# Optimization experiments

Measured on AMD Instinct MI355X. Metric: run time of the kernel, lower is better.

The kernel has to match this reference:

```python
import jax, jax.numpy as jnp
import numpy as np
from jax import lax

CAPACITY = 32768
KEY_SIZE = 64
VALUE_SIZE = 64
BATCH = 4096


def setup_inputs() -> dict:
    key = jax.random.key(0)
    ks = jax.random.split(key, 9)
    inp = {
        "keys": jax.random.normal(ks[0], (BATCH, KEY_SIZE), dtype=jnp.float32),
        "values": jax.random.normal(ks[1], (BATCH, VALUE_SIZE), dtype=jnp.float32),
        "query": jax.random.normal(ks[2], (BATCH, KEY_SIZE), dtype=jnp.float32),
        # learned memory tables (init as torch.randn * 0.01)
        "mem_keys": jax.random.normal(ks[3], (CAPACITY, KEY_SIZE), dtype=jnp.float32) * 0.01,
        "mem_values": jax.random.normal(ks[4], (CAPACITY, VALUE_SIZE), dtype=jnp.float32) * 0.01,
        # nn.Linear params (fan-in uniform init approximation)
        "Wk": jax.random.uniform(ks[5], (KEY_SIZE, KEY_SIZE), jnp.float32, -1, 1) / np.sqrt(KEY_SIZE),
        "bk": jax.random.uniform(ks[6], (KEY_SIZE,), jnp.float32, -1, 1) / np.sqrt(KEY_SIZE),
        "Wv": jax.random.uniform(ks[7], (VALUE_SIZE, VALUE_SIZE), jnp.float32, -1, 1) / np.sqrt(VALUE_SIZE),
        "bv": jax.random.uniform(ks[8], (VALUE_SIZE,), jnp.float32, -1, 1) / np.sqrt(VALUE_SIZE),
    }
    return inp


def reference(keys, values, query, mem_keys, mem_values, Wk, bk, Wv, bv):
    # NOTE: forward() calls self.store(keys, query): `query` is stored as the
    # values, and the `values` arg is never used. Reproduced faithfully.
    batch = keys.shape[0]
    capacity = mem_keys.shape[0]

    # ---- store ----
    keys_proj = jnp.tanh(keys @ Wk.T + bk)                      # [B, K]
    sim = keys_proj @ mem_keys.T                                # [B, cap] (big)
    # argmax of softmax == argmax of logits
    top_match = jnp.argmax(sim, axis=-1)                        # [B]
    stored_vals = jnp.tanh(query @ Wv.T + bv)                   # [B, V]

    # matching the sequential Python loop in the original.
    winner = jnp.full((capacity,), -1, dtype=jnp.int32).at[top_match].max(
        jnp.arange(batch, dtype=jnp.int32))                     # [cap]
    written = (winner >= 0)[:, None]
    safe_winner = jnp.clip(winner, 0, batch - 1)
    # .detach() in original -> stop_gradient on written entries
    new_keys = jnp.where(written, lax.stop_gradient(keys_proj)[safe_winner], mem_keys)
    new_values = jnp.where(written, lax.stop_gradient(stored_vals)[safe_winner], mem_values)

    # ---- retrieve ----
    query_proj = jnp.tanh(query @ Wk.T + bk)                    # [B, K]
    attention = jax.nn.softmax(query_proj @ new_keys.T, axis=-1)  # [B, cap]
    retrieved = attention @ new_values                          # [B, V]
    return retrieved, attention
```

## Files before the change

### kernel.cpp

```cpp
#include <hip/hip_runtime.h>
#include <math.h>
#include <float.h>

#define BATCH 4096
#define CAP   32768

typedef _Float16 f16;
typedef _Float16 f16x8 __attribute__((ext_vector_type(8)));
typedef float    f32x4 __attribute__((ext_vector_type(4)));

__device__ __forceinline__ f32x4 MF(f16x8 a, f16x8 b, f32x4 c) {
    return __builtin_amdgcn_mfma_f32_16x16x32_f16(a, b, c, 0, 0, 0);
}

__global__ __launch_bounds__(256) void prep_kernel(
    const float* __restrict__ keys, const float* __restrict__ query,
    const float* __restrict__ Wk, const float* __restrict__ bk,
    const float* __restrict__ Wv, const float* __restrict__ bv,
    const float* __restrict__ mk,
    f16* __restrict__ kph, f16* __restrict__ kpl,
    f16* __restrict__ svh,
    f16* __restrict__ qph, f16* __restrict__ qpl,
    f16* __restrict__ mkh, f16* __restrict__ mkl,
    int* __restrict__ winner)
{
    int bx = blockIdx.x;
    int tid = threadIdx.x;
    if (bx >= 768) {
        int i = (bx - 768)*256 + tid;
        float x = mk[i];
        f16 h = (f16)x;
        mkh[i] = h;
        mkl[i] = (f16)((x - (float)h) * 2048.0f);
        if (i < CAP) winner[i] = -1;
        return;
    }
    int job = bx >> 8;
    const float *in, *W, *b; f16 *oh, *ol; bool scaled;
    if (job == 0)      { in = keys;  W = Wk; b = bk; oh = kph; ol = kpl;     scaled = true;  }
    else if (job == 1) { in = query; W = Wv; b = bv; oh = svh; ol = nullptr; scaled = false; }
    else               { in = query; W = Wk; b = bk; oh = qph; ol = qpl;     scaled = false; }

    __shared__ float Wl[64*65];
    __shared__ float inl[16*65];
    __shared__ float bl[64];
    int row0 = (bx & 255) * 16;
    for (int i = tid; i < 4096; i += 256) { int r = i >> 6, c = i & 63; Wl[r*65+c] = W[i]; }
    for (int i = tid; i < 1024; i += 256) { int r = i >> 6, c = i & 63; inl[r*65+c] = in[(row0+r)*64 + c]; }
    if (tid < 64) bl[tid] = b[tid];
    __syncthreads();

    int col = tid & 63;
    int rq  = tid >> 6;
    #pragma unroll
    for (int q = 0; q < 4; ++q) {
        int r = rq*4 + q;
        float acc = bl[col];
        #pragma unroll
        for (int k = 0; k < 64; ++k) acc += inl[r*65+k] * Wl[col*65+k];
        float t = tanhf(acc);
        f16 h = (f16)t;
        oh[(row0+r)*64 + col] = h;
        if (ol) {
            float lo = t - (float)h;
            if (scaled) lo *= 2048.0f;
            ol[(row0+r)*64 + col] = (f16)lo;
        }
    }
}

__global__ __launch_bounds__(256, 2) void sim_kernel(
    const f16* __restrict__ Aph, const f16* __restrict__ Apl,
    const f16* __restrict__ Bph, const f16* __restrict__ Bpl,
    float* __restrict__ bestv, int* __restrict__ besti)
{
    __shared__ __align__(16) f16 Bh[64*72], Bl[64*72];
    int tid = threadIdx.x, l = tid & 63, w = tid >> 6;
    int sb = blockIdx.x, rb = blockIdx.y;
    int row0 = rb*256 + w*64;
    int lr = l & 15, lg = l >> 4;
    int sl0 = tid >> 3, ch = tid & 7;

    f16x8 ah[4][2], al[4][2];
    #pragma unroll
    for (int i = 0; i < 4; ++i)
        #pragma unroll
        for (int t = 0; t < 2; ++t) {
            size_t o = (size_t)(row0 + i*16 + lr)*64 + t*32 + lg*8;
            ah[i][t] = *(const f16x8*)&Aph[o];
            al[i][t] = *(const f16x8*)&Apl[o];
        }
    float bvv[4][4]; int bii[4][4];
    #pragma unroll
    for (int i = 0; i < 4; ++i)
        #pragma unroll
        for (int j = 0; j < 4; ++j) { bvv[i][j] = -FLT_MAX; bii[i][j] = 0; }

    f16x8 pb[2][2];
    {
        int s0 = sb*1024;
        pb[0][0] = *(const f16x8*)&Bph[(size_t)(s0+sl0)*64 + ch*8];
        pb[0][1] = *(const f16x8*)&Bpl[(size_t)(s0+sl0)*64 + ch*8];
        pb[1][0] = *(const f16x8*)&Bph[(size_t)(s0+sl0+32)*64 + ch*8];
        pb[1][1] = *(const f16x8*)&Bpl[(size_t)(s0+sl0+32)*64 + ch*8];
    }

    for (int st = 0; st < 16; ++st) {
        int s0 = sb*1024 + st*64;
        __syncthreads();
        *(f16x8*)&Bh[sl0*72 + ch*8]      = pb[0][0];
        *(f16x8*)&Bl[sl0*72 + ch*8]      = pb[0][1];
        *(f16x8*)&Bh[(sl0+32)*72 + ch*8] = pb[1][0];
        *(f16x8*)&Bl[(sl0+32)*72 + ch*8] = pb[1][1];
        __syncthreads();
        if (st + 1 < 16) {
            int sn = s0 + 64;
            pb[0][0] = *(const f16x8*)&Bph[(size_t)(sn+sl0)*64 + ch*8];
            pb[0][1] = *(const f16x8*)&Bpl[(size_t)(sn+sl0)*64 + ch*8];
            pb[1][0] = *(const f16x8*)&Bph[(size_t)(sn+sl0+32)*64 + ch*8];
            pb[1][1] = *(const f16x8*)&Bpl[(size_t)(sn+sl0+32)*64 + ch*8];
        }
        #pragma unroll
        for (int cf = 0; cf < 4; ++cf) {
            int c0 = cf*16;
            f16x8 bh[2], bl2[2];
            #pragma unroll
            for (int t = 0; t < 2; ++t) {
                bh[t]  = *(const f16x8*)&Bh[(c0+lr)*72 + t*32 + lg*8];
                bl2[t] = *(const f16x8*)&Bl[(c0+lr)*72 + t*32 + lg*8];
            }
            f32x4 z = {0.f,0.f,0.f,0.f};
            f32x4 aA[4] = {z,z,z,z}, aB[4] = {z,z,z,z};
            #pragma unroll
            for (int i = 0; i < 4; ++i)
                #pragma unroll
                for (int t = 0; t < 2; ++t) {
                    aA[i] = MF(ah[i][t], bh[t],  aA[i]);
                    aB[i] = MF(ah[i][t], bl2[t], aB[i]);
                    aB[i] = MF(al[i][t], bh[t],  aB[i]);
                }
            int slot = s0 + c0 + lr;
            #pragma unroll
            for (int i = 0; i < 4; ++i)
                #pragma unroll
                for (int j = 0; j < 4; ++j) {
                    float v = aA[i][j] + aB[i][j]*(1.0f/2048.0f);
                    if (v > bvv[i][j]) { bvv[i][j] = v; bii[i][j] = slot; }
                }
        }
    }
    #pragma unroll
    for (int m = 1; m < 16; m <<= 1)
        #pragma unroll
        for (int i = 0; i < 4; ++i)
            #pragma unroll
            for (int j = 0; j < 4; ++j) {
                float ov = __shfl_xor(bvv[i][j], m);
                int   oi = __shfl_xor(bii[i][j], m);
                if (ov > bvv[i][j] || (ov == bvv[i][j] && oi < bii[i][j])) { bvv[i][j] = ov; bii[i][j] = oi; }
            }
    if (lr == 0) {
        #pragma unroll
        for (int i = 0; i < 4; ++i)
            #pragma unroll
            for (int j = 0; j < 4; ++j) {
                int r = row0 + i*16 + lg*4 + j;
                bestv[r*32 + sb] = bvv[i][j];
                besti[r*32 + sb] = bii[i][j];
            }
    }
}

__global__ void argmax_scatter_kernel(const float* __restrict__ bestv,
                                      const int* __restrict__ besti,
                                      int* __restrict__ winner)
{
    int r = blockIdx.x*256 + threadIdx.x;
    if (r >= BATCH) return;
    float bv = bestv[r*32]; int bi = besti[r*32];
    #pragma unroll
    for (int sb = 1; sb < 32; ++sb) {
        float v = bestv[r*32+sb]; int ii = besti[r*32+sb];
        if (v > bv || (v == bv && ii < bi)) { bv = v; bi = ii; }
    }
    atomicMax(&winner[bi], r);
}

__global__ __launch_bounds__(256) void build_kernel(
    const int* __restrict__ winner,
    const f16* __restrict__ kph, const f16* __restrict__ kpl,
    const f16* __restrict__ svh,
    const float* __restrict__ mk, const float* __restrict__ mv,
    f16* __restrict__ nkh, f16* __restrict__ nkl,
    f16* __restrict__ nvTh)
{
    __shared__ __align__(16) f16 Lh[64*72];
    int tid = threadIdx.x;
    int s0 = blockIdx.x*64;
    #pragma unroll
    for (int c = 0; c < 2; ++c) {
        int task = tid + 256*c; int sl = task >> 3, ch = task & 7;
        int s = s0 + sl; int w = winner[s];
        f16x8 hk, lk, hv;
        if (w >= 0) {
            hk = *(const f16x8*)&kph[(size_t)w*64 + ch*8];
            f16x8 lraw = *(const f16x8*)&kpl[(size_t)w*64 + ch*8];
            #pragma unroll
            for (int q = 0; q < 8; ++q) lk[q] = (f16)((float)lraw[q] * (1.0f/2048.0f));
            hv = *(const f16x8*)&svh[(size_t)w*64 + ch*8];
        } else {
            #pragma unroll
            for (int q = 0; q < 8; ++q) {
                float x = mk[(size_t)s*64 + ch*8 + q];
                f16 h = (f16)x; hk[q] = h; lk[q] = (f16)(x - (float)h);
                float y = mv[(size_t)s*64 + ch*8 + q];
                hv[q] = (f16)y;
            }
        }
        *(f16x8*)&nkh[(size_t)s*64 + ch*8] = hk;
        *(f16x8*)&nkl[(size_t)s*64 + ch*8] = lk;
        *(f16x8*)&Lh[sl*72 + ch*8] = hv;
    }
    __syncthreads();
    int v = tid >> 2, sc = (tid & 3)*16;
    f16x8 a, b2;
    #pragma unroll
    for (int q = 0; q < 8; ++q) { a[q] = Lh[(sc+q)*72 + v]; b2[q] = Lh[(sc+8+q)*72 + v]; }
    *(f16x8*)&nvTh[(size_t)v*CAP + s0 + sc]     = a;
    *(f16x8*)&nvTh[(size_t)v*CAP + s0 + sc + 8] = b2;
}

__global__ __launch_bounds__(256, 2) void logits_stats_kernel(
    const f16* __restrict__ Aph,
    const f16* __restrict__ Bph,
    float* __restrict__ s_part)
{
    __shared__ __align__(16) f16 Bh[64*72];
    int tid = threadIdx.x, l = tid & 63, w = tid >> 6;
    int sb = blockIdx.x, rb = blockIdx.y;
    int row0 = rb*512 + w*128;
    int lr = l & 15, lg = l >> 4;
    int sl0 = tid >> 3, ch = tid & 7;

    f16x8 ah[8][2];
    #pragma unroll
    for (int i = 0; i < 8; ++i)
        #pragma unroll
        for (int t = 0; t < 2; ++t)
            ah[i][t] = *(const f16x8*)&Aph[(size_t)(row0 + i*16 + lr)*64 + t*32 + lg*8];

    float ssum[8][4];
    #pragma unroll
    for (int i = 0; i < 8; ++i)
        #pragma unroll
        for (int j = 0; j < 4; ++j) ssum[i][j] = 0.f;

    f16x8 pb[2];
    {
        int s0 = sb*512;
        pb[0] = *(const f16x8*)&Bph[(size_t)(s0+sl0)*64 + ch*8];
        pb[1] = *(const f16x8*)&Bph[(size_t)(s0+sl0+32)*64 + ch*8];
    }

    for (int st = 0; st < 8; ++st) {
        int s0 = sb*512 + st*64;
        __syncthreads();
        *(f16x8*)&Bh[sl0*72 + ch*8]      = pb[0];
        *(f16x8*)&Bh[(sl0+32)*72 + ch*8] = pb[1];
        __syncthreads();
        if (st + 1 < 8) {
            int sn = s0 + 64;
            pb[0] = *(const f16x8*)&Bph[(size_t)(sn+sl0)*64 + ch*8];
            pb[1] = *(const f16x8*)&Bph[(size_t)(sn+sl0+32)*64 + ch*8];
        }
        #pragma unroll
        for (int cf = 0; cf < 4; ++cf) {
            int c0 = cf*16;
            f16x8 bh[2];
            #pragma unroll
            for (int t = 0; t < 2; ++t)
                bh[t] = *(const f16x8*)&Bh[(c0+lr)*72 + t*32 + lg*8];
            f32x4 z = {0.f,0.f,0.f,0.f};
            f32x4 acc[8] = {z,z,z,z,z,z,z,z};
            #pragma unroll
            for (int i = 0; i < 8; ++i) {
                acc[i] = MF(ah[i][0], bh[0], acc[i]);
                acc[i] = MF(ah[i][1], bh[1], acc[i]);
            }
            #pragma unroll
            for (int i = 0; i < 8; ++i)
                #pragma unroll
                for (int j = 0; j < 4; ++j)
                    ssum[i][j] += __expf(acc[i][j]);
        }
    }
    #pragma unroll
    for (int m = 1; m < 16; m <<= 1)
        #pragma unroll
        for (int i = 0; i < 8; ++i)
            #pragma unroll
            for (int j = 0; j < 4; ++j)
                ssum[i][j] += __shfl_xor(ssum[i][j], m);
    if (lr == 0) {
        #pragma unroll
        for (int i = 0; i < 8; ++i)
            #pragma unroll
            for (int j = 0; j < 4; ++j) {
                int r = row0 + i*16 + lg*4 + j;
                s_part[r*64 + sb] = ssum[i][j];
            }
    }
}

__global__ __launch_bounds__(256, 2) void pass2_kernel(
    const f16* __restrict__ qph, const f16* __restrict__ qpl,
    const f16* __restrict__ nkh,
    const f16* __restrict__ nvTh,
    const float* __restrict__ s_part,
    float* __restrict__ att, float* __restrict__ ret_part)
{
    __shared__ __align__(16) f16 Kh[64*72];
    __shared__ __align__(16) f16 Vh[64*72];
    __shared__ __align__(16) f16 Ph[4][64*72];
    __shared__ float iSl[256];
    int tid = threadIdx.x, l = tid & 63, w = tid >> 6;
    int sb = blockIdx.x, rb = blockIdx.y;
    int brow0 = rb*256;
    int wrow0 = brow0 + w*64;
    int lr = l & 15, lg = l >> 4;
    int sl0 = tid >> 3, ch = tid & 7;
    f16* Pw = &Ph[w][0];

    {
        const float4* p = (const float4*)(s_part + (size_t)(brow0 + tid)*64);
        float S = 0.f;
        #pragma unroll
        for (int q = 0; q < 16; ++q) {
            float4 v = p[q];
            S += (v.x + v.y) + (v.z + v.w);
        }
        iSl[tid] = 1.0f / S;
    }

    f16x8 ah[4][2], al[4][2];
    #pragma unroll
    for (int i = 0; i < 4; ++i)
        #pragma unroll
        for (int t = 0; t < 2; ++t) {
            size_t o = (size_t)(wrow0 + i*16 + lr)*64 + t*32 + lg*8;
            ah[i][t] = *(const f16x8*)&qph[o];
            al[i][t] = *(const f16x8*)&qpl[o];
        }
    f16x8 pk[2], pv[2];
    {
        int s0g = sb*1024;
        pk[0] = *(const f16x8*)&nkh[(size_t)(s0g+sl0)*64 + ch*8];
        pk[1] = *(const f16x8*)&nkh[(size_t)(s0g+sl0+32)*64 + ch*8];
        pv[0] = *(const f16x8*)&nvTh[(size_t)sl0*CAP + s0g + ch*8];
        pv[1] = *(const f16x8*)&nvTh[(size_t)(sl0+32)*CAP + s0g + ch*8];
    }
    __syncthreads();
    float iS[4][4];
    #pragma unroll
    for (int i = 0; i < 4; ++i)
        #pragma unroll
        for (int j = 0; j < 4; ++j)
            iS[i][j] = iSl[w*64 + i*16 + lg*4 + j];

    f32x4 z = {0.f,0.f,0.f,0.f};
    f32x4 pacc[4][4] = {{z,z,z,z},{z,z,z,z},{z,z,z,z},{z,z,z,z}};

    for (int st = 0; st < 16; ++st) {
        int s0g = sb*1024 + st*64;
        __syncthreads();
        *(f16x8*)&Kh[sl0*72 + ch*8]      = pk[0];
        *(f16x8*)&Kh[(sl0+32)*72 + ch*8] = pk[1];
        *(f16x8*)&Vh[sl0*72 + ch*8]      = pv[0];
        *(f16x8*)&Vh[(sl0+32)*72 + ch*8] = pv[1];
        __syncthreads();
        if (st + 1 < 16) {
            int sn = s0g + 64;
            pk[0] = *(const f16x8*)&nkh[(size_t)(sn+sl0)*64 + ch*8];
            pk[1] = *(const f16x8*)&nkh[(size_t)(sn+sl0+32)*64 + ch*8];
            pv[0] = *(const f16x8*)&nvTh[(size_t)sl0*CAP + sn + ch*8];
            pv[1] = *(const f16x8*)&nvTh[(size_t)(sl0+32)*CAP + sn + ch*8];
        }
        #pragma unroll
        for (int cf = 0; cf < 4; ++cf) {
            int c0 = cf*16;
            f16x8 bh[2];
            #pragma unroll
            for (int t = 0; t < 2; ++t)
                bh[t] = *(const f16x8*)&Kh[(c0+lr)*72 + t*32 + lg*8];
            f32x4 qacc[4] = {z,z,z,z};
            #pragma unroll
            for (int i = 0; i < 4; ++i)
                #pragma unroll
                for (int t = 0; t < 2; ++t) {
                    qacc[i] = MF(ah[i][t], bh[t], qacc[i]);
                    qacc[i] = MF(al[i][t], bh[t], qacc[i]);
                }
            #pragma unroll
            for (int i = 0; i < 4; ++i)
                #pragma unroll
                for (int j = 0; j < 4; ++j) {
                    float a = __expf(qacc[i][j]) * iS[i][j];
                    Pw[(i*16 + lg*4 + j)*72 + c0 + lr] = (f16)a;
                }
        }
        asm volatile("s_waitcnt lgkmcnt(0)" ::: "memory");
        f16x8 pah[4][2];
        #pragma unroll
        for (int i = 0; i < 4; ++i)
            #pragma unroll
            for (int t = 0; t < 2; ++t)
                pah[i][t] = *(const f16x8*)&Pw[(i*16 + lr)*72 + t*32 + lg*8];
        #pragma unroll
        for (int vf = 0; vf < 4; ++vf) {
            f16x8 vbh[2];
            #pragma unroll
            for (int t = 0; t < 2; ++t)
                vbh[t] = *(const f16x8*)&Vh[(vf*16 + lr)*72 + t*32 + lg*8];
            #pragma unroll
            for (int i = 0; i < 4; ++i)
                #pragma unroll
                for (int t = 0; t < 2; ++t)
                    pacc[i][vf] = MF(pah[i][t], vbh[t], pacc[i][vf]);
        }
        #pragma unroll
        for (int it = 0; it < 8; ++it) {
            int rloc = it*8 + (l >> 3);
            int k0 = (l & 7)*8;
            f16x8 ph = *(const f16x8*)&Pw[rloc*72 + k0];
            f32x4 lo = {(float)ph[0], (float)ph[1], (float)ph[2], (float)ph[3]};
            f32x4 hi = {(float)ph[4], (float)ph[5], (float)ph[6], (float)ph[7]};
            float* dst = &att[(size_t)(wrow0 + rloc)*CAP + s0g + k0];
            *(f32x4*)dst = lo;
            *(f32x4*)(dst + 4) = hi;
        }
    }
    #pragma unroll
    for (int i = 0; i < 4; ++i)
        #pragma unroll
        for (int vf = 0; vf < 4; ++vf)
            #pragma unroll
            for (int j = 0; j < 4; ++j) {
                int gr = wrow0 + i*16 + lg*4 + j;
                int gc = vf*16 + lr;
                ret_part[((size_t)sb*BATCH + gr)*64 + gc] = pacc[i][vf][j];
            }
}

__global__ void ret_reduce_kernel(const float* __restrict__ rp, float* __restrict__ out)
{
    int i4 = blockIdx.x*256 + threadIdx.x;
    float4 s = {0.f,0.f,0.f,0.f};
    #pragma unroll
    for (int sb = 0; sb < 32; ++sb) {
        float4 p = ((const float4*)(rp + (size_t)sb*BATCH*64))[i4];
        s.x += p.x; s.y += p.y; s.z += p.z; s.w += p.w;
    }
    ((float4*)out)[i4] = s;
}

extern "C" void kernel_launch(void* const* d_in, const int* in_sizes, int n_in,
                              void* d_out, int out_size, void* d_ws, size_t ws_size,
                              hipStream_t stream) {
    const float* keys       = (const float*)d_in[0];
    const float* query      = (const float*)d_in[2];
    const float* mem_keys   = (const float*)d_in[3];
    const float* mem_values = (const float*)d_in[4];
    const float* Wk         = (const float*)d_in[5];
    const float* bk         = (const float*)d_in[6];
    const float* Wv         = (const float*)d_in[7];
    const float* bv         = (const float*)d_in[8];

    float* out = (float*)d_out;
    float* ret = out;
    float* att = out + BATCH*64;

    char* ws = (char*)d_ws;
    const size_t SK = (size_t)BATCH*64*2;
    const size_t SC = (size_t)CAP*64*2;
    f16* kph  = (f16*)(ws + 0*SK);
    f16* kpl  = (f16*)(ws + 1*SK);
    f16* svh  = (f16*)(ws + 2*SK);
    f16* qph  = (f16*)(ws + 3*SK);
    f16* qpl  = (f16*)(ws + 4*SK);
    size_t o = 5*SK;
    f16* nkh  = (f16*)(ws + o);            o += SC;
    f16* nkl  = (f16*)(ws + o);            o += SC;
    f16* nvTh = (f16*)(ws + o);            o += SC;
    float* bestv  = (float*)(ws + o);      o += (size_t)BATCH*32*4;
    int*   besti  = (int*)(ws + o);        o += (size_t)BATCH*32*4;
    float* s_part = (float*)(ws + o);      o += (size_t)BATCH*64*4;
    int*   winner = (int*)(ws + o);        o += (size_t)CAP*4;
    float* ret_part = (float*)(ws + o);
    f16* mkh = (f16*)ret_part;
    f16* mkl = (f16*)((char*)ret_part + SC);

    prep_kernel<<<768 + CAP*64/256, 256, 0, stream>>>(
        keys, query, Wk, bk, Wv, bv, mem_keys,
        kph, kpl, svh, qph, qpl, mkh, mkl, winner);
    sim_kernel<<<dim3(32, 16), 256, 0, stream>>>(kph, kpl, mkh, mkl, bestv, besti);
    argmax_scatter_kernel<<<BATCH/256, 256, 0, stream>>>(bestv, besti, winner);
    build_kernel<<<CAP/64, 256, 0, stream>>>(
        winner, kph, kpl, svh, mem_keys, mem_values, nkh, nkl, nvTh);
    logits_stats_kernel<<<dim3(64, 8), 256, 0, stream>>>(qph, nkh, s_part);
    pass2_kernel<<<dim3(32, 16), 256, 0, stream>>>(
        qph, qpl, nkh, nvTh, s_part, att, ret_part);
    ret_reduce_kernel<<<BATCH*64/4/256, 256, 0, stream>>>(ret_part, ret);
}
```

Before: 303.4 us.

## Drop LDS staging in sim and pass2, halve row tiles, remove unused nkl

The sim and pass2 kernels stop staging memory key/value tiles through shared memory with double-buffered prefetch and barriers. They now load MFMA B operands straight from global memory (relying on L1/L2). Each warp handles 32 rows instead of 64, which doubles the grid and raises the occupancy hints. The unused low-precision new-key buffer nkl is removed from build_kernel. This trades LDS traffic and syncs for more global/cache loads and less B-operand reuse per block.

```diff
diff --git a/kernel.cpp b/kernel.cpp
--- a/kernel.cpp
+++ b/kernel.cpp
@@ -69,70 +69,47 @@
     }
 }
 
-__global__ __launch_bounds__(256, 2) void sim_kernel(
+__global__ __launch_bounds__(256, 4) void sim_kernel(
     const f16* __restrict__ Aph, const f16* __restrict__ Apl,
     const f16* __restrict__ Bph, const f16* __restrict__ Bpl,
     float* __restrict__ bestv, int* __restrict__ besti)
 {
-    __shared__ __align__(16) f16 Bh[64*72], Bl[64*72];
     int tid = threadIdx.x, l = tid & 63, w = tid >> 6;
     int sb = blockIdx.x, rb = blockIdx.y;
-    int row0 = rb*256 + w*64;
+    int row0 = rb*128 + w*32;
     int lr = l & 15, lg = l >> 4;
-    int sl0 = tid >> 3, ch = tid & 7;
-
-    f16x8 ah[4][2], al[4][2];
-    #pragma unroll
-    for (int i = 0; i < 4; ++i)
+
+    f16x8 ah[2][2], al[2][2];
+    #pragma unroll
+    for (int i = 0; i < 2; ++i)
         #pragma unroll
         for (int t = 0; t < 2; ++t) {
             size_t o = (size_t)(row0 + i*16 + lr)*64 + t*32 + lg*8;
             ah[i][t] = *(const f16x8*)&Aph[o];
             al[i][t] = *(const f16x8*)&Apl[o];
         }
-    float bvv[4][4]; int bii[4][4];
-    #pragma unroll
-    for (int i = 0; i < 4; ++i)
+    float bvv[2][4]; int bii[2][4];
+    #pragma unroll
+    for (int i = 0; i < 2; ++i)
         #pragma unroll
         for (int j = 0; j < 4; ++j) { bvv[i][j] = -FLT_MAX; bii[i][j] = 0; }
-
-    f16x8 pb[2][2];
-    {
-        int s0 = sb*1024;
-        pb[0][0] = *(const f16x8*)&Bph[(size_t)(s0+sl0)*64 + ch*8];
-        pb[0][1] = *(const f16x8*)&Bpl[(size_t)(s0+sl0)*64 + ch*8];
-        pb[1][0] = *(const f16x8*)&Bph[(size_t)(s0+sl0+32)*64 + ch*8];
-        pb[1][1] = *(const f16x8*)&Bpl[(size_t)(s0+sl0+32)*64 + ch*8];
-    }
 
     for (int st = 0; st < 16; ++st) {
         int s0 = sb*1024 + st*64;
-        __syncthreads();
-        *(f16x8*)&Bh[sl0*72 + ch*8]      = pb[0][0];
-        *(f16x8*)&Bl[sl0*72 + ch*8]      = pb[0][1];
-        *(f16x8*)&Bh[(sl0+32)*72 + ch*8] = pb[1][0];
-        *(f16x8*)&Bl[(sl0+32)*72 + ch*8] = pb[1][1];
-        __syncthreads();
-        if (st + 1 < 16) {
-            int sn = s0 + 64;
-            pb[0][0] = *(const f16x8*)&Bph[(size_t)(sn+sl0)*64 + ch*8];
-            pb[0][1] = *(const f16x8*)&Bpl[(size_t)(sn+sl0)*64 + ch*8];
-            pb[1][0] = *(const f16x8*)&Bph[(size_t)(sn+sl0+32)*64 + ch*8];
-            pb[1][1] = *(const f16x8*)&Bpl[(size_t)(sn+sl0+32)*64 + ch*8];
-        }
         #pragma unroll
         for (int cf = 0; cf < 4; ++cf) {
             int c0 = cf*16;
             f16x8 bh[2], bl2[2];
             #pragma unroll
             for (int t = 0; t < 2; ++t) {
-                bh[t]  = *(const f16x8*)&Bh[(c0+lr)*72 + t*32 + lg*8];
-                bl2[t] = *(const f16x8*)&Bl[(c0+lr)*72 + t*32 + lg*8];
+                size_t o = (size_t)(s0 + c0 + lr)*64 + t*32 + lg*8;
+                bh[t]  = *(const f16x8*)&Bph[o];
+                bl2[t] = *(const f16x8*)&Bpl[o];
             }
             f32x4 z = {0.f,0.f,0.f,0.f};
-            f32x4 aA[4] = {z,z,z,z}, aB[4] = {z,z,z,z};
-            #pragma unroll
-            for (int i = 0; i < 4; ++i)
+            f32x4 aA[2] = {z,z}, aB[2] = {z,z};
+            #pragma unroll
+            for (int i = 0; i < 2; ++i)
                 #pragma unroll
                 for (int t = 0; t < 2; ++t) {
                     aA[i] = MF(ah[i][t], bh[t],  aA[i]);
@@ -141,7 +118,7 @@
                 }
             int slot = s0 + c0 + lr;
             #pragma unroll
-            for (int i = 0; i < 4; ++i)
+            for (int i = 0; i < 2; ++i)
                 #pragma unroll
                 for (int j = 0; j < 4; ++j) {
                     float v = aA[i][j] + aB[i][j]*(1.0f/2048.0f);
@@ -152,7 +129,7 @@
     #pragma unroll
     for (int m = 1; m < 16; m <<= 1)
         #pragma unroll
-        for (int i = 0; i < 4; ++i)
+        for (int i = 0; i < 2; ++i)
             #pragma unroll
             for (int j = 0; j < 4; ++j) {
                 float ov = __shfl_xor(bvv[i][j], m);
@@ -161,7 +138,7 @@
             }
     if (lr == 0) {
         #pragma unroll
-        for (int i = 0; i < 4; ++i)
+        for (int i = 0; i < 2; ++i)
             #pragma unroll
             for (int j = 0; j < 4; ++j) {
                 int r = row0 + i*16 + lg*4 + j;
@@ -188,10 +165,10 @@
 
 __global__ __launch_bounds__(256) void build_kernel(
     const int* __restrict__ winner,
-    const f16* __restrict__ kph, const f16* __restrict__ kpl,
+    const f16* __restrict__ kph,
     const f16* __restrict__ svh,
     const float* __restrict__ mk, const float* __restrict__ mv,
-    f16* __restrict__ nkh, f16* __restrict__ nkl,
+    f16* __restrict__ nkh,
     f16* __restrict__ nvTh)
 {
     __shared__ __align__(16) f16 Lh[64*72];
@@ -201,24 +178,18 @@
     for (int c = 0; c < 2; ++c) {
         int task = tid + 256*c; int sl = task >> 3, ch = task & 7;
         int s = s0 + sl; int w = winner[s];
-        f16x8 hk, lk, hv;
+        f16x8 hk, hv;
         if (w >= 0) {
             hk = *(const f16x8*)&kph[(size_t)w*64 + ch*8];
-            f16x8 lraw = *(const f16x8*)&kpl[(size_t)w*64 + ch*8];
-            #pragma unroll
-            for (int q = 0; q < 8; ++q) lk[q] = (f16)((float)lraw[q] * (1.0f/2048.0f));
             hv = *(const f16x8*)&svh[(size_t)w*64 + ch*8];
         } else {
             #pragma unroll
             for (int q = 0; q < 8; ++q) {
-                float x = mk[(size_t)s*64 + ch*8 + q];
-                f16 h = (f16)x; hk[q] = h; lk[q] = (f16)(x - (float)h);
-                float y = mv[(size_t)s*64 + ch*8 + q];
-                hv[q] = (f16)y;
+                hk[q] = (f16)mk[(size_t)s*64 + ch*8 + q];
+                hv[q] = (f16)mv[(size_t)s*64 + ch*8 + q];
             }
         }
         *(f16x8*)&nkh[(size_t)s*64 + ch*8] = hk;
-        *(f16x8*)&nkl[(size_t)s*64 + ch*8] = lk;
         *(f16x8*)&Lh[sl*72 + ch*8] = hv;
     }
     __syncthreads();
@@ -312,96 +283,74 @@
     }
 }
 
-__global__ __launch_bounds__(256, 2) void pass2_kernel(
+__global__ __launch_bounds__(256, 3) void pass2_kernel(
     const f16* __restrict__ qph, const f16* __restrict__ qpl,
     const f16* __restrict__ nkh,
     const f16* __restrict__ nvTh,
     const float* __restrict__ s_part,
     float* __restrict__ att, float* __restrict__ ret_part)
 {
-    __shared__ __align__(16) f16 Kh[64*72];
-    __shared__ __align__(16) f16 Vh[64*72];
-    __shared__ __align__(16) f16 Ph[4][64*72];
-    __shared__ float iSl[256];
+    __shared__ __align__(16) f16 Ph[4][32*72];
+    __shared__ float iSl[128];
     int tid = threadIdx.x, l = tid & 63, w = tid >> 6;
     int sb = blockIdx.x, rb = blockIdx.y;
-    int brow0 = rb*256;
-    int wrow0 = brow0 + w*64;
+    int brow0 = rb*128;
+    int wrow0 = brow0 + w*32;
     int lr = l & 15, lg = l >> 4;
-    int sl0 = tid >> 3, ch = tid & 7;
     f16* Pw = &Ph[w][0];
 
     {
-        const float4* p = (const float4*)(s_part + (size_t)(brow0 + tid)*64);
+        int r_loc = tid >> 1, half = tid & 1;
+        const float4* p = (const float4*)(s_part + (size_t)(brow0 + r_loc)*64 + half*32);
         float S = 0.f;
         #pragma unroll
-        for (int q = 0; q < 16; ++q) {
+        for (int q = 0; q < 8; ++q) {
             float4 v = p[q];
             S += (v.x + v.y) + (v.z + v.w);
         }
-        iSl[tid] = 1.0f / S;
-    }
-
-    f16x8 ah[4][2], al[4][2];
-    #pragma unroll
-    for (int i = 0; i < 4; ++i)
+        S += __shfl_xor(S, 1);
+        if (!half) iSl[r_loc] = 1.0f / S;
+    }
+    __syncthreads();
+
+    f16x8 ah[2][2], al[2][2];
+    #pragma unroll
+    for (int i = 0; i < 2; ++i)
         #pragma unroll
         for (int t = 0; t < 2; ++t) {
             size_t o = (size_t)(wrow0 + i*16 + lr)*64 + t*32 + lg*8;
             ah[i][t] = *(const f16x8*)&qph[o];
             al[i][t] = *(const f16x8*)&qpl[o];
         }
-    f16x8 pk[2], pv[2];
-    {
-        int s0g = sb*1024;
-        pk[0] = *(const f16x8*)&nkh[(size_t)(s0g+sl0)*64 + ch*8];
-        pk[1] = *(const f16x8*)&nkh[(size_t)(s0g+sl0+32)*64 + ch*8];
-        pv[0] = *(const f16x8*)&nvTh[(size_t)sl0*CAP + s0g + ch*8];
-        pv[1] = *(const f16x8*)&nvTh[(size_t)(sl0+32)*CAP + s0g + ch*8];
-    }
-    __syncthreads();
-    float iS[4][4];
-    #pragma unroll
-    for (int i = 0; i < 4; ++i)
+    float iS[2][4];
+    #pragma unroll
+    for (int i = 0; i < 2; ++i)
         #pragma unroll
         for (int j = 0; j < 4; ++j)
-            iS[i][j] = iSl[w*64 + i*16 + lg*4 + j];
+            iS[i][j] = iSl[w*32 + i*16 + lg*4 + j];
 
     f32x4 z = {0.f,0.f,0.f,0.f};
-    f32x4 pacc[4][4] = {{z,z,z,z},{z,z,z,z},{z,z,z,z},{z,z,z,z}};
+    f32x4 pacc[2][4] = {{z,z,z,z},{z,z,z,z}};
 
     for (int st = 0; st < 16; ++st) {
         int s0g = sb*1024 + st*64;
-        __syncthreads();
-        *(f16x8*)&Kh[sl0*72 + ch*8]      = pk[0];
-        *(f16x8*)&Kh[(sl0+32)*72 + ch*8] = pk[1];
-        *(f16x8*)&Vh[sl0*72 + ch*8]      = pv[0];
-        *(f16x8*)&Vh[(sl0+32)*72 + ch*8] = pv[1];
-        __syncthreads();
-        if (st + 1 < 16) {
-            int sn = s0g + 64;
-            pk[0] = *(const f16x8*)&nkh[(size_t)(sn+sl0)*64 + ch*8];
-            pk[1] = *(const f16x8*)&nkh[(size_t)(sn+sl0+32)*64 + ch*8];
-            pv[0] = *(const f16x8*)&nvTh[(size_t)sl0*CAP + sn + ch*8];
-            pv[1] = *(const f16x8*)&nvTh[(size_t)(sl0+32)*CAP + sn + ch*8];
-        }
         #pragma unroll
         for (int cf = 0; cf < 4; ++cf) {
             int c0 = cf*16;
             f16x8 bh[2];
             #pragma unroll
             for (int t = 0; t < 2; ++t)
-                bh[t] = *(const f16x8*)&Kh[(c0+lr)*72 + t*32 + lg*8];
-            f32x4 qacc[4] = {z,z,z,z};
-            #pragma unroll
-            for (int i = 0; i < 4; ++i)
+                bh[t] = *(const f16x8*)&nkh[(size_t)(s0g + c0 + lr)*64 + t*32 + lg*8];
+            f32x4 qacc[2] = {z,z};
+            #pragma unroll
+            for (int i = 0; i < 2; ++i)
                 #pragma unroll
                 for (int t = 0; t < 2; ++t) {
                     qacc[i] = MF(ah[i][t], bh[t], qacc[i]);
                     qacc[i] = MF(al[i][t], bh[t], qacc[i]);
                 }
             #pragma unroll
-            for (int i = 0; i < 4; ++i)
+            for (int i = 0; i < 2; ++i)
                 #pragma unroll
                 for (int j = 0; j < 4; ++j) {
                     float a = __expf(qacc[i][j]) * iS[i][j];
@@ -409,9 +358,9 @@
                 }
         }
         asm volatile("s_waitcnt lgkmcnt(0)" ::: "memory");
-        f16x8 pah[4][2];
-        #pragma unroll
-        for (int i = 0; i < 4; ++i)
+        f16x8 pah[2][2];
+        #pragma unroll
+        for (int i = 0; i < 2; ++i)
             #pragma unroll
             for (int t = 0; t < 2; ++t)
                 pah[i][t] = *(const f16x8*)&Pw[(i*16 + lr)*72 + t*32 + lg*8];
@@ -420,15 +369,15 @@
             f16x8 vbh[2];
             #pragma unroll
             for (int t = 0; t < 2; ++t)
-                vbh[t] = *(const f16x8*)&Vh[(vf*16 + lr)*72 + t*32 + lg*8];
-            #pragma unroll
-            for (int i = 0; i < 4; ++i)
+                vbh[t] = *(const f16x8*)&nvTh[(size_t)(vf*16 + lr)*CAP + s0g + t*32 + lg*8];
+            #pragma unroll
+            for (int i = 0; i < 2; ++i)
                 #pragma unroll
                 for (int t = 0; t < 2; ++t)
                     pacc[i][vf] = MF(pah[i][t], vbh[t], pacc[i][vf]);
         }
         #pragma unroll
-        for (int it = 0; it < 8; ++it) {
+        for (int it = 0; it < 4; ++it) {
             int rloc = it*8 + (l >> 3);
             int k0 = (l & 7)*8;
             f16x8 ph = *(const f16x8*)&Pw[rloc*72 + k0];
@@ -440,7 +389,7 @@
         }
     }
     #pragma unroll
-    for (int i = 0; i < 4; ++i)
+    for (int i = 0; i < 2; ++i)
         #pragma unroll
         for (int vf = 0; vf < 4; ++vf)
             #pragma unroll
@@ -489,7 +438,6 @@
     f16* qpl  = (f16*)(ws + 4*SK);
     size_t o = 5*SK;
     f16* nkh  = (f16*)(ws + o);            o += SC;
-    f16* nkl  = (f16*)(ws + o);            o += SC;
     f16* nvTh = (f16*)(ws + o);            o += SC;
     float* bestv  = (float*)(ws + o);      o += (size_t)BATCH*32*4;
     int*   besti  = (int*)(ws + o);        o += (size_t)BATCH*32*4;
@@ -502,12 +450,12 @@
     prep_kernel<<<768 + CAP*64/256, 256, 0, stream>>>(
         keys, query, Wk, bk, Wv, bv, mem_keys,
         kph, kpl, svh, qph, qpl, mkh, mkl, winner);
-    sim_kernel<<<dim3(32, 16), 256, 0, stream>>>(kph, kpl, mkh, mkl, bestv, besti);
+    sim_kernel<<<dim3(32, 32), 256, 0, stream>>>(kph, kpl, mkh, mkl, bestv, besti);
     argmax_scatter_kernel<<<BATCH/256, 256, 0, stream>>>(bestv, besti, winner);
     build_kernel<<<CAP/64, 256, 0, stream>>>(
-        winner, kph, kpl, svh, mem_keys, mem_values, nkh, nkl, nvTh);
+        winner, kph, svh, mem_keys, mem_values, nkh, nvTh);
     logits_stats_kernel<<<dim3(64, 8), 256, 0, stream>>>(qph, nkh, s_part);
-    pass2_kernel<<<dim3(32, 16), 256, 0, stream>>>(
+    pass2_kernel<<<dim3(32, 32), 256, 0, stream>>>(
         qph, qpl, nkh, nvTh, s_part, att, ret_part);
     ret_reduce_kernel<<<BATCH*64/4/256, 256, 0, stream>>>(ret_part, ret);
 }
```

Result: slower. 491.7 us (+62.1%).
